# Optimization experiments

Hardware: AMD Instinct MI355X
Metric: run time of the kernel (lower is better)

The kernel has to match this reference:

```python
import jax, jax.numpy as jnp
import numpy as np

C, CH, H = 128, 32, 4  # c_in, c_hidden, n_head


def _layer_norm(x, w, b, eps=1e-5):
    mu = jnp.mean(x, axis=-1, keepdims=True)
    var = jnp.var(x, axis=-1, keepdims=True)
    return (x - mu) * jax.lax.rsqrt(var + eps) * w + b


def _tri_attn(x, ln_w, ln_b, wq, wk, wv, wz, wg, bg, wo, bo):
    # x: [B, I, J, C]; attention runs over J independently for each row I
    B, I, J, _ = x.shape
    x = _layer_norm(x, ln_w, ln_b)
    q = (x @ wq).reshape(B, I, J, H, CH) * (CH ** -0.5)
    k = (x @ wk).reshape(B, I, J, H, CH)
    v = (x @ wv).reshape(B, I, J, H, CH)
    # learned pairwise triangle bias: [B, I, J, H] -> [B, 1, H, I, J]
    tb = jnp.transpose(x @ wz, (0, 3, 1, 2))[:, None]
    scores = jnp.einsum('biqhd,bikhd->bihqk', q, k) + tb  # [B, I, H, J, J]
    a = jax.nn.softmax(scores, axis=-1)
    o = jnp.einsum('bihqk,bikhd->biqhd', a, v)
    g = jax.nn.sigmoid(x @ wg + bg).reshape(B, I, J, H, CH)
    o = (o * g).reshape(B, I, J, H * CH)
    return o @ wo + bo


def setup_inputs() -> dict:
    key = jax.random.key(0)
    ks = jax.random.split(key, 16)
    B, N = 1, 256
    inp = {'cmap': jax.random.normal(ks[0], (B, C, N, N), jnp.float32)}
    for i, p in enumerate(['s', 'e']):
        kq, kk, kv, kz, kg, ko = jax.random.split(ks[1 + i], 6)
        sd = 0.02
        inp[p + '_ln_w'] = jnp.ones((C,), jnp.float32)
        inp[p + '_ln_b'] = jnp.zeros((C,), jnp.float32)
        inp[p + '_wq'] = jax.random.normal(kq, (C, H * CH), jnp.float32) * sd
        inp[p + '_wk'] = jax.random.normal(kk, (C, H * CH), jnp.float32) * sd
        inp[p + '_wv'] = jax.random.normal(kv, (C, H * CH), jnp.float32) * sd
        inp[p + '_wz'] = jax.random.normal(kz, (C, H), jnp.float32) * sd
        inp[p + '_wg'] = jax.random.normal(kg, (C, H * CH), jnp.float32) * sd
        inp[p + '_bg'] = jnp.ones((H * CH,), jnp.float32)  # gating bias init = 1
        inp[p + '_wo'] = jax.random.normal(ko, (H * CH, C), jnp.float32) * sd
        inp[p + '_bo'] = jnp.zeros((C,), jnp.float32)
    return inp


def reference(cmap,
              s_ln_w, s_ln_b, s_wq, s_wk, s_wv, s_wz, s_wg, s_bg, s_wo, s_bo,
              e_ln_w, e_ln_b, e_wq, e_wk, e_wv, e_wz, e_wg, e_bg, e_wo, e_bo):
    # cmap: [B, C, I, J] -> channels last [B, I, J, C]
    x = jnp.transpose(cmap, (0, 2, 3, 1))
    # triangle attention around starting node (dropout is identity in eval)
    x = x + _tri_attn(x, s_ln_w, s_ln_b, s_wq, s_wk, s_wv, s_wz, s_wg, s_bg, s_wo, s_bo)
    # triangle attention around ending node: transpose I<->J, attend, transpose back
    xt = jnp.swapaxes(x, 1, 2)
    x = x + jnp.swapaxes(
        _tri_attn(xt, e_ln_w, e_ln_b, e_wq, e_wk, e_wv, e_wz, e_wg, e_bg, e_wo, e_bo), 1, 2)
    return jnp.transpose(x, (0, 3, 1, 2))
```

## Files before the change

kernel.cpp:

```cpp
#include <hip/hip_runtime.h>
#include <hip/hip_bf16.h>

#define NNX 256
#define CCX 128
#define HHX 4
#define CHDX 32
#define NIJ (NNX*NNX)

typedef __hip_bfloat16 bf16;
typedef __hip_bfloat162 bf162;
typedef __attribute__((ext_vector_type(8))) short short8v;
typedef __attribute__((ext_vector_type(4))) float float4v;
typedef __attribute__((ext_vector_type(4))) unsigned int uint4v;

__device__ __forceinline__ float4v MFMA(short8v a, short8v b, float4v c){
  return __builtin_amdgcn_mfma_f32_16x16x32_bf16(a, b, c, 0, 0, 0);
}

__device__ __forceinline__ unsigned pk2(float a, float b){
  unsigned short ua = __bfloat16_as_ushort(__float2bfloat16(a));
  unsigned short ub = __bfloat16_as_ushort(__float2bfloat16(b));
  return (unsigned)ua | ((unsigned)ub << 16);
}
__device__ __forceinline__ float ubf(unsigned short u){
  return __bfloat162float(__ushort_as_bfloat16(u));
}

__device__ __forceinline__ void load8bf16(const bf16* p, float* f){
  const bf162* p2 = (const bf162*)p;
  #pragma unroll
  for(int t=0;t<4;++t){ float2 xy = __bfloat1622float2(p2[t]); f[2*t]=xy.x; f[2*t+1]=xy.y; }
}

__global__ __launch_bounds__(256) void k_tin(const float* __restrict__ in, float* __restrict__ out){
  __shared__ float t[32][33];
  const int i = blockIdx.z, jt = blockIdx.x, ct = blockIdx.y;
  const int tx = threadIdx.x, ty = threadIdx.y;
  #pragma unroll
  for(int k=0;k<32;k+=8){
    int c = ct*32 + ty + k;
    t[ty+k][tx] = in[(size_t)c*NIJ + (size_t)i*NNX + jt*32 + tx];
  }
  __syncthreads();
  #pragma unroll
  for(int k=0;k<32;k+=8){
    int j = jt*32 + ty + k;
    out[((size_t)i*NNX + j)*CCX + ct*32 + tx] = t[tx][ty+k];
  }
}

__global__ __launch_bounds__(256) void k_tout(const float* __restrict__ x, float* __restrict__ out){
  __shared__ float t[32][33];
  const int i = blockIdx.z, jt = blockIdx.x, ct = blockIdx.y;
  const int tx = threadIdx.x, ty = threadIdx.y;
  #pragma unroll
  for(int k=0;k<32;k+=8){
    t[ty+k][tx] = x[((size_t)i*NNX + jt*32+ty+k)*CCX + ct*32 + tx];
  }
  __syncthreads();
  #pragma unroll
  for(int k=0;k<32;k+=8){
    out[(size_t)(ct*32+ty+k)*NIJ + (size_t)i*NNX + jt*32 + tx] = t[tx][ty+k];
  }
}

template<int TRANS>
__global__ __launch_bounds__(256) void k_lntb(const float* __restrict__ x,
    const float* __restrict__ w, const float* __restrict__ b,
    const float* __restrict__ wz, bf16* __restrict__ xln, float* __restrict__ tb2){
  const int r = blockIdx.x*4 + threadIdx.y;
  const int ii = r>>8, jj = r&255;
  const float* src = x + (size_t)(TRANS ? (jj*NNX+ii) : r)*CCX;
  const int c = threadIdx.x*2;
  float2 v = *(const float2*)(src+c);
  float s = v.x+v.y, s2 = v.x*v.x+v.y*v.y;
  #pragma unroll
  for(int off=32; off>0; off>>=1){ s += __shfl_xor(s,off); s2 += __shfl_xor(s2,off); }
  float mu = s*0.0078125f;
  float var = s2*0.0078125f - mu*mu;
  float rs = rsqrtf(var+1e-5f);
  float a0 = (v.x-mu)*rs*w[c]+b[c];
  float a1 = (v.y-mu)*rs*w[c+1]+b[c+1];
  bf162 hp; hp.x = __float2bfloat16(a0); hp.y = __float2bfloat16(a1);
  *(bf162*)(xln + (size_t)r*CCX + c) = hp;
  float acc[4];
  #pragma unroll
  for(int hh=0;hh<4;++hh) acc[hh] = a0*wz[c*4+hh] + a1*wz[(c+1)*4+hh];
  #pragma unroll
  for(int off=32; off>0; off>>=1){
    #pragma unroll
    for(int hh=0;hh<4;++hh) acc[hh] += __shfl_xor(acc[hh], off);
  }
  if(threadIdx.x==0){
    #pragma unroll
    for(int hh=0;hh<4;++hh) tb2[(size_t)hh*NIJ + r] = acc[hh];
  }
}

__global__ __launch_bounds__(256) void k_cvtw(const float* __restrict__ wq,
    const float* __restrict__ wk, const float* __restrict__ wv,
    const float* __restrict__ wg, const float* __restrict__ wo, bf16* __restrict__ wT){
  int idx = blockIdx.x*256 + threadIdx.x;
  if(idx < 65536){
    int n = idx >> 7, k = idx & 127;
    const float* W = (n<128)?wq:(n<256)?wk:(n<384)?wv:wg;
    wT[idx] = __float2bfloat16(W[k*CCX + (n&127)]);
  } else {
    int idx2 = idx - 65536;
    int n = idx2 >> 7, k = idx2 & 127;
    wT[idx] = __float2bfloat16(wo[k*CCX + n]);
  }
}

__global__ __launch_bounds__(256,2) void k_fattn(const bf16* __restrict__ xln,
    const bf16* __restrict__ wT, const float* __restrict__ bg,
    const float* __restrict__ tb2, bf16* __restrict__ op){
  __shared__ unsigned short Qs[256*40];
  __shared__ unsigned short Ks[256*40];
  __shared__ unsigned short Vt[32*256];
  const int id = blockIdx.x;
  const int i = id >> 2, h = id & 3;
  const int tid = threadIdx.x;
  const int w = tid >> 6, l = tid & 63;
  const int lq = l & 15, g = l >> 4;
  const int mb = w*64;

  short8v bx[4][4];
  #pragma unroll
  for(int ms=0; ms<4; ++ms){
    const size_t row = (size_t)i*NNX + mb + ms*16 + lq;
    #pragma unroll
    for(int kc=0; kc<4; ++kc)
      bx[ms][kc] = *(const short8v*)(xln + row*CCX + kc*32 + g*8);
  }
  float4v greg[2][4];
  char* qsb = (char*)Qs;
  char* ksb = (char*)Ks;
  char* vtb = (char*)Vt;
  #pragma unroll
  for(int mat=0; mat<4; ++mat){
    #pragma unroll
    for(int half=0; half<2; ++half){
      const int n0 = mat*128 + h*32 + half*16;
      float4v acc[4];
      #pragma unroll
      for(int ms=0; ms<4; ++ms) acc[ms] = (float4v)(0.f);
      #pragma unroll
      for(int kc=0; kc<4; ++kc){
        short8v aw = *(const short8v*)(wT + (size_t)(n0 + lq)*CCX + kc*32 + g*8);
        #pragma unroll
        for(int ms=0; ms<4; ++ms) acc[ms] = MFMA(aw, bx[ms][kc], acc[ms]);
      }
      if(mat==0){
        #pragma unroll
        for(int ms=0; ms<4; ++ms){
          const int row = mb + ms*16 + lq;
          uint2 pw; pw.x = pk2(acc[ms][0]*0.17677669529663687f, acc[ms][1]*0.17677669529663687f);
                    pw.y = pk2(acc[ms][2]*0.17677669529663687f, acc[ms][3]*0.17677669529663687f);
          *(uint2*)(qsb + (size_t)row*80 + half*32 + g*8) = pw;
        }
      } else if(mat==1){
        #pragma unroll
        for(int ms=0; ms<4; ++ms){
          const int row = mb + ms*16 + lq;
          uint2 pw; pw.x = pk2(acc[ms][0], acc[ms][1]);
                    pw.y = pk2(acc[ms][2], acc[ms][3]);
          *(uint2*)(ksb + (size_t)row*80 + half*32 + g*8) = pw;
        }
      } else if(mat==2){
        #pragma unroll
        for(int ms=0; ms<4; ++ms){
          const int k = mb + ms*16 + lq;
          const int j = k & 31;
          const int kap = (k & ~31) + 8*((j>>2)&3) + 4*((j>>4)&1) + (j&3);
          #pragma unroll
          for(int r=0; r<4; ++r){
            const int d = half*16 + 4*g + r;
            const int off = d*512 + ((2*kap) ^ ((d&7)<<4));
            *(unsigned short*)(vtb + off) = __bfloat16_as_ushort(__float2bfloat16(acc[ms][r]));
          }
        }
      } else {
        const float4 bg4 = *(const float4*)(bg + h*32 + half*16 + 4*g);
        #pragma unroll
        for(int ms=0; ms<4; ++ms){
          float4v t = acc[ms];
          t[0]+=bg4.x; t[1]+=bg4.y; t[2]+=bg4.z; t[3]+=bg4.w;
          greg[half][ms] = t;
        }
      }
    }
  }
  __syncthreads();

  bf16* obh = op + ((size_t)h*NIJ + (size_t)i*NNX)*CHDX;
  #pragma unroll 1
  for(int sub=0; sub<4; ++sub){
    const int q0 = mb + sub*16;
    const int q  = q0 + lq;
    short8v qf = *(const short8v*)(qsb + (size_t)q*80 + g*16);
    const float* tbq = tb2 + (size_t)h*NIJ + (size_t)q*NNX;
    float4v s[16];
    #pragma unroll
    for(int t=0;t<16;++t){
      short8v ak = *(const short8v*)(ksb + (size_t)(t*16 + lq)*80 + g*16);
      float4v bb = *(const float4v*)(tbq + t*16 + g*4);
      s[t] = MFMA(ak, qf, bb);
    }
    float m = -1e30f;
    #pragma unroll
    for(int t=0;t<16;++t)
      m = fmaxf(m, fmaxf(fmaxf(s[t][0], s[t][1]), fmaxf(s[t][2], s[t][3])));
    m = fmaxf(m, __shfl_xor(m,16));
    m = fmaxf(m, __shfl_xor(m,32));
    float lsum = 0.f;
    #pragma unroll
    for(int t=0;t<16;++t){
      #pragma unroll
      for(int r=0;r<4;++r){ float e = __expf(s[t][r]-m); s[t][r]=e; lsum+=e; }
    }
    lsum += __shfl_xor(lsum,16);
    lsum += __shfl_xor(lsum,32);
    const float linv = 1.0f/lsum;
    #pragma unroll
    for(int dt=0; dt<2; ++dt){
      float4v acc = (float4v)(0.f);
      #pragma unroll
      for(int c=0;c<8;++c){
        const int vrow = dt*16 + lq;
        short8v av = *(const short8v*)(vtb + (size_t)vrow*512 + ((16*g + 64*c) ^ ((vrow&7)<<4)));
        uint4 pb;
        pb.x = pk2(s[2*c][0],   s[2*c][1]);
        pb.y = pk2(s[2*c][2],   s[2*c][3]);
        pb.z = pk2(s[2*c+1][0], s[2*c+1][1]);
        pb.w = pk2(s[2*c+1][2], s[2*c+1][3]);
        short8v bp;
        bp[0]=(short)(pb.x&0xffff); bp[1]=(short)(pb.x>>16);
        bp[2]=(short)(pb.y&0xffff); bp[3]=(short)(pb.y>>16);
        bp[4]=(short)(pb.z&0xffff); bp[5]=(short)(pb.z>>16);
        bp[6]=(short)(pb.w&0xffff); bp[7]=(short)(pb.w>>16);
        acc = MFMA(av, bp, acc);
      }
      const float4v gg = greg[dt][sub];
      float o0 = acc[0]*linv / (1.f + __expf(-gg[0]));
      float o1 = acc[1]*linv / (1.f + __expf(-gg[1]));
      float o2 = acc[2]*linv / (1.f + __expf(-gg[2]));
      float o3 = acc[3]*linv / (1.f + __expf(-gg[3]));
      uint2 pw; pw.x = pk2(o0,o1); pw.y = pk2(o2,o3);
      *(uint2*)(ksb + (size_t)(mb + lq*4 + 2*dt + (g>>1))*80 + 64 + (g&1)*8) = pw;
    }
    {
      const int r2 = l >> 2, c2 = l & 3;
      uint4v ow = *(const uint4v*)(ksb + (size_t)(mb + r2*4 + c2)*80 + 64);
      __builtin_nontemporal_store(ow, (uint4v*)(obh + (size_t)(q0 + r2)*CHDX + c2*8));
    }
  }
}

template<int TRANS>
__global__ __launch_bounds__(256) void k_oprojm(const bf16* __restrict__ ob,
    const bf16* __restrict__ woT, const float* __restrict__ bo, float* __restrict__ x){
  const int tid = threadIdx.x;
  const int w = tid >> 6, l = tid & 63;
  const int lq = l & 15, g = l >> 4;
  const int mbase = blockIdx.x*128 + w*32;
  short8v bx[2][4];
  #pragma unroll
  for(int ms=0; ms<2; ++ms){
    const size_t mrow = mbase + ms*16 + lq;
    #pragma unroll
    for(int kc=0; kc<4; ++kc)
      bx[ms][kc] = *(const short8v*)(ob + ((size_t)kc*NIJ + mrow)*CHDX + g*8);
  }
  #pragma unroll
  for(int nj=0; nj<8; ++nj){
    float4v acc0 = (float4v)(0.f), acc1 = (float4v)(0.f);
    #pragma unroll
    for(int kc=0; kc<4; ++kc){
      short8v aw = *(const short8v*)(woT + (size_t)(nj*16 + lq)*CCX + kc*32 + g*8);
      acc0 = MFMA(aw, bx[0][kc], acc0);
      acc1 = MFMA(aw, bx[1][kc], acc1);
    }
    const int col = nj*16 + 4*g;
    const float4 bo4 = *(const float4*)(bo + col);
    #pragma unroll
    for(int ms=0; ms<2; ++ms){
      const int r = mbase + ms*16 + lq;
      const int ii = r>>8, jj = r&255;
      float* dst = x + (size_t)(TRANS ? (jj*NNX+ii) : r)*CCX + col;
      float4 xv = *(float4*)dst;
      xv.x += ((ms==0)?acc0[0]:acc1[0]) + bo4.x;
      xv.y += ((ms==0)?acc0[1]:acc1[1]) + bo4.y;
      xv.z += ((ms==0)?acc0[2]:acc1[2]) + bo4.z;
      xv.w += ((ms==0)?acc0[3]:acc1[3]) + bo4.w;
      *(float4*)dst = xv;
    }
  }
}

extern "C" void kernel_launch(void* const* d_in, const int* in_sizes, int n_in,
                              void* d_out, int out_size, void* d_ws, size_t ws_size,
                              hipStream_t stream){
  const float* cmap = (const float*)d_in[0];
  char* ws = (char*)d_ws;
  float* x   = (float*)(ws);
  bf16* xln  = (bf16*)(ws + 33554432);
  bf16* ob   = (bf16*)(ws + 50331648);
  float* tb2 = (float*)(ws + 117440512);
  bf16* wT   = (bf16*)d_out;
  bf16* woT  = wT + 65536;
  float* outp = (float*)d_out;

  k_tin<<<dim3(8,4,NNX), dim3(32,8), 0, stream>>>(cmap, x);

  for(int p=0;p<2;++p){
    const int b = 1 + 10*p;
    const float* lnw = (const float*)d_in[b+0];
    const float* lnb = (const float*)d_in[b+1];
    const float* wq  = (const float*)d_in[b+2];
    const float* wk  = (const float*)d_in[b+3];
    const float* wv  = (const float*)d_in[b+4];
    const float* wz  = (const float*)d_in[b+5];
    const float* wg  = (const float*)d_in[b+6];
    const float* bg  = (const float*)d_in[b+7];
    const float* wo  = (const float*)d_in[b+8];
    const float* bo  = (const float*)d_in[b+9];

    k_cvtw<<<320, 256, 0, stream>>>(wq, wk, wv, wg, wo, wT);

    if(p==0) k_lntb<0><<<NIJ/4, dim3(64,4), 0, stream>>>(x, lnw, lnb, wz, xln, tb2);
    else     k_lntb<1><<<NIJ/4, dim3(64,4), 0, stream>>>(x, lnw, lnb, wz, xln, tb2);

    k_fattn<<<1024, 256, 0, stream>>>(xln, wT, bg, tb2, ob);

    if(p==0) k_oprojm<0><<<NIJ/128, 256, 0, stream>>>(ob, woT, bo, x);
    else     k_oprojm<1><<<NIJ/128, 256, 0, stream>>>(ob, woT, bo, x);
  }

  k_tout<<<dim3(8,4,NNX), dim3(32,8), 0, stream>>>(x, outp);
}
```

Measured before the change: 240.0 us.

## Keep Q fragments in registers via shuffles, raise occupancy, reorder blocks by head

Removes the Q shared-memory buffer by building the Q MFMA operand fragments directly in registers with cross-lane shuffles. The gate values are stored packed as bf16 instead of fp32 to cut register use, and launch bounds go from 2 to 4 blocks per CU. Block indexing becomes head-major, so consecutive blocks share a head's bias plane, and s_setprio raises priority around the MFMA loops. The sub-tile loop is fully unrolled through a template. Risks include register spills at the higher occupancy target and slightly lower gate precision from the bf16 packing.

Result: slower. 250.3 us (+4.3%).

```diff
diff --git a/kernel.cpp b/kernel.cpp
--- a/kernel.cpp
+++ b/kernel.cpp
@@ -112,19 +112,93 @@
   }
 }
 
-__global__ __launch_bounds__(256,2) void k_fattn(const bf16* __restrict__ xln,
+template<int SUB>
+__device__ __forceinline__ void attn_sub(const int mb,
+    const int lq, const int g, const int l,
+    short8v qf, uint2 pgl, uint2 pgh,
+    char* ksb, const char* vtb, const float* tbq_base, bf16* __restrict__ obh){
+  const int q0 = mb + SUB*16;
+  const int q  = q0 + lq;
+  const float* tbq = tbq_base + (size_t)q*NNX;
+  float4v s[16];
+  __builtin_amdgcn_s_setprio(1);
+  #pragma unroll
+  for(int t=0;t<16;++t){
+    short8v ak = *(const short8v*)(ksb + (size_t)(t*16 + lq)*80 + g*16);
+    float4v bb = *(const float4v*)(tbq + t*16 + g*4);
+    s[t] = MFMA(ak, qf, bb);
+  }
+  __builtin_amdgcn_s_setprio(0);
+  float m = -1e30f;
+  #pragma unroll
+  for(int t=0;t<16;++t)
+    m = fmaxf(m, fmaxf(fmaxf(s[t][0], s[t][1]), fmaxf(s[t][2], s[t][3])));
+  m = fmaxf(m, __shfl_xor(m,16));
+  m = fmaxf(m, __shfl_xor(m,32));
+  float lsum = 0.f;
+  #pragma unroll
+  for(int t=0;t<16;++t){
+    #pragma unroll
+    for(int r=0;r<4;++r){ float e = __expf(s[t][r]-m); s[t][r]=e; lsum+=e; }
+  }
+  lsum += __shfl_xor(lsum,16);
+  lsum += __shfl_xor(lsum,32);
+  const float linv = 1.0f/lsum;
+  #pragma unroll
+  for(int dt=0; dt<2; ++dt){
+    float4v acc = (float4v)(0.f);
+    __builtin_amdgcn_s_setprio(1);
+    #pragma unroll
+    for(int c=0;c<8;++c){
+      const int vrow = dt*16 + lq;
+      short8v av = *(const short8v*)(vtb + (size_t)vrow*512 + ((16*g + 64*c) ^ ((vrow&7)<<4)));
+      uint4 pb;
+      pb.x = pk2(s[2*c][0],   s[2*c][1]);
+      pb.y = pk2(s[2*c][2],   s[2*c][3]);
+      pb.z = pk2(s[2*c+1][0], s[2*c+1][1]);
+      pb.w = pk2(s[2*c+1][2], s[2*c+1][3]);
+      short8v bp;
+      bp[0]=(short)(pb.x&0xffff); bp[1]=(short)(pb.x>>16);
+      bp[2]=(short)(pb.y&0xffff); bp[3]=(short)(pb.y>>16);
+      bp[4]=(short)(pb.z&0xffff); bp[5]=(short)(pb.z>>16);
+      bp[6]=(short)(pb.w&0xffff); bp[7]=(short)(pb.w>>16);
+      acc = MFMA(av, bp, acc);
+    }
+    __builtin_amdgcn_s_setprio(0);
+    const uint2 pg = dt ? pgh : pgl;
+    float g0 = ubf((unsigned short)(pg.x & 0xffff));
+    float g1 = ubf((unsigned short)(pg.x >> 16));
+    float g2 = ubf((unsigned short)(pg.y & 0xffff));
+    float g3 = ubf((unsigned short)(pg.y >> 16));
+    float o0 = acc[0]*linv / (1.f + __expf(-g0));
+    float o1 = acc[1]*linv / (1.f + __expf(-g1));
+    float o2 = acc[2]*linv / (1.f + __expf(-g2));
+    float o3 = acc[3]*linv / (1.f + __expf(-g3));
+    uint2 pw; pw.x = pk2(o0,o1); pw.y = pk2(o2,o3);
+    *(uint2*)(ksb + (size_t)(mb + lq*4 + 2*dt + (g>>1))*80 + 64 + (g&1)*8) = pw;
+  }
+  {
+    const int r2 = l >> 2, c2 = l & 3;
+    uint4v ow = *(const uint4v*)(ksb + (size_t)(mb + r2*4 + c2)*80 + 64);
+    __builtin_nontemporal_store(ow, (uint4v*)(obh + (size_t)(q0 + r2)*CHDX + c2*8));
+  }
+}
+
+__global__ __launch_bounds__(256,4) void k_fattn(const bf16* __restrict__ xln,
     const bf16* __restrict__ wT, const float* __restrict__ bg,
     const float* __restrict__ tb2, bf16* __restrict__ op){
-  __shared__ unsigned short Qs[256*40];
   __shared__ unsigned short Ks[256*40];
   __shared__ unsigned short Vt[32*256];
   const int id = blockIdx.x;
-  const int i = id >> 2, h = id & 3;
+  const int h = id >> 8, i = id & 255;
   const int tid = threadIdx.x;
   const int w = tid >> 6, l = tid & 63;
   const int lq = l & 15, g = l >> 4;
   const int mb = w*64;
 
+  char* ksb = (char*)Ks;
+  char* vtb = (char*)Vt;
+
   short8v bx[4][4];
   #pragma unroll
   for(int ms=0; ms<4; ++ms){
@@ -133,15 +207,15 @@
     for(int kc=0; kc<4; ++kc)
       bx[ms][kc] = *(const short8v*)(xln + row*CCX + kc*32 + g*8);
   }
-  float4v greg[2][4];
-  char* qsb = (char*)Qs;
-  char* ksb = (char*)Ks;
-  char* vtb = (char*)Vt;
-  #pragma unroll
-  for(int mat=0; mat<4; ++mat){
+
+  uint4v qfr[4];
+  uint2 pgl[4], pgh[4];
+
+  {
+    uint2 pqa[4][2];
     #pragma unroll
     for(int half=0; half<2; ++half){
-      const int n0 = mat*128 + h*32 + half*16;
+      const int n0 = h*32 + half*16;
       float4v acc[4];
       #pragma unroll
       for(int ms=0; ms<4; ++ms) acc[ms] = (float4v)(0.f);
@@ -151,110 +225,100 @@
         #pragma unroll
         for(int ms=0; ms<4; ++ms) acc[ms] = MFMA(aw, bx[ms][kc], acc[ms]);
       }
-      if(mat==0){
-        #pragma unroll
-        for(int ms=0; ms<4; ++ms){
-          const int row = mb + ms*16 + lq;
-          uint2 pw; pw.x = pk2(acc[ms][0]*0.17677669529663687f, acc[ms][1]*0.17677669529663687f);
-                    pw.y = pk2(acc[ms][2]*0.17677669529663687f, acc[ms][3]*0.17677669529663687f);
-          *(uint2*)(qsb + (size_t)row*80 + half*32 + g*8) = pw;
-        }
-      } else if(mat==1){
-        #pragma unroll
-        for(int ms=0; ms<4; ++ms){
-          const int row = mb + ms*16 + lq;
-          uint2 pw; pw.x = pk2(acc[ms][0], acc[ms][1]);
-                    pw.y = pk2(acc[ms][2], acc[ms][3]);
-          *(uint2*)(ksb + (size_t)row*80 + half*32 + g*8) = pw;
-        }
-      } else if(mat==2){
-        #pragma unroll
-        for(int ms=0; ms<4; ++ms){
-          const int k = mb + ms*16 + lq;
-          const int j = k & 31;
-          const int kap = (k & ~31) + 8*((j>>2)&3) + 4*((j>>4)&1) + (j&3);
-          #pragma unroll
-          for(int r=0; r<4; ++r){
-            const int d = half*16 + 4*g + r;
-            const int off = d*512 + ((2*kap) ^ ((d&7)<<4));
-            *(unsigned short*)(vtb + off) = __bfloat16_as_ushort(__float2bfloat16(acc[ms][r]));
-          }
-        }
-      } else {
-        const float4 bg4 = *(const float4*)(bg + h*32 + half*16 + 4*g);
-        #pragma unroll
-        for(int ms=0; ms<4; ++ms){
-          float4v t = acc[ms];
-          t[0]+=bg4.x; t[1]+=bg4.y; t[2]+=bg4.z; t[3]+=bg4.w;
-          greg[half][ms] = t;
-        }
+      #pragma unroll
+      for(int ms=0; ms<4; ++ms){
+        pqa[ms][half].x = pk2(acc[ms][0]*0.17677669529663687f, acc[ms][1]*0.17677669529663687f);
+        pqa[ms][half].y = pk2(acc[ms][2]*0.17677669529663687f, acc[ms][3]*0.17677669529663687f);
       }
     }
+    const int srcA = lq + 32*(g&1);
+    const int hsel = g >> 1;
+    #pragma unroll
+    for(int ms=0; ms<4; ++ms){
+      unsigned sx = hsel ? pqa[ms][1].x : pqa[ms][0].x;
+      unsigned sy = hsel ? pqa[ms][1].y : pqa[ms][0].y;
+      qfr[ms].x = __shfl(sx, srcA);
+      qfr[ms].y = __shfl(sy, srcA);
+      qfr[ms].z = __shfl(sx, srcA+16);
+      qfr[ms].w = __shfl(sy, srcA+16);
+    }
+  }
+
+  #pragma unroll
+  for(int half=0; half<2; ++half){
+    const int n0 = 128 + h*32 + half*16;
+    float4v acc[4];
+    #pragma unroll
+    for(int ms=0; ms<4; ++ms) acc[ms] = (float4v)(0.f);
+    #pragma unroll
+    for(int kc=0; kc<4; ++kc){
+      short8v aw = *(const short8v*)(wT + (size_t)(n0 + lq)*CCX + kc*32 + g*8);
+      #pragma unroll
+      for(int ms=0; ms<4; ++ms) acc[ms] = MFMA(aw, bx[ms][kc], acc[ms]);
+    }
+    #pragma unroll
+    for(int ms=0; ms<4; ++ms){
+      const int row = mb + ms*16 + lq;
+      uint2 pw; pw.x = pk2(acc[ms][0], acc[ms][1]);
+                pw.y = pk2(acc[ms][2], acc[ms][3]);
+      *(uint2*)(ksb + (size_t)row*80 + half*32 + g*8) = pw;
+    }
+  }
+
+  #pragma unroll
+  for(int half=0; half<2; ++half){
+    const int n0 = 256 + h*32 + half*16;
+    float4v acc[4];
+    #pragma unroll
+    for(int ms=0; ms<4; ++ms) acc[ms] = (float4v)(0.f);
+    #pragma unroll
+    for(int kc=0; kc<4; ++kc){
+      short8v aw = *(const short8v*)(wT + (size_t)(n0 + lq)*CCX + kc*32 + g*8);
+      #pragma unroll
+      for(int ms=0; ms<4; ++ms) acc[ms] = MFMA(aw, bx[ms][kc], acc[ms]);
+    }
+    #pragma unroll
+    for(int ms=0; ms<4; ++ms){
+      const int k = mb + ms*16 + lq;
+      const int j = k & 31;
+      const int kap = (k & ~31) + 8*((j>>2)&3) + 4*((j>>4)&1) + (j&3);
+      #pragma unroll
+      for(int r=0; r<4; ++r){
+        const int d = half*16 + 4*g + r;
+        const int off = d*512 + ((2*kap) ^ ((d&7)<<4));
+        *(unsigned short*)(vtb + off) = __bfloat16_as_ushort(__float2bfloat16(acc[ms][r]));
+      }
+    }
+  }
+
+  #pragma unroll
+  for(int half=0; half<2; ++half){
+    const int n0 = 384 + h*32 + half*16;
+    float4v acc[4];
+    #pragma unroll
+    for(int ms=0; ms<4; ++ms) acc[ms] = (float4v)(0.f);
+    #pragma unroll
+    for(int kc=0; kc<4; ++kc){
+      short8v aw = *(const short8v*)(wT + (size_t)(n0 + lq)*CCX + kc*32 + g*8);
+      #pragma unroll
+      for(int ms=0; ms<4; ++ms) acc[ms] = MFMA(aw, bx[ms][kc], acc[ms]);
+    }
+    const float4 bg4 = *(const float4*)(bg + h*32 + half*16 + 4*g);
+    #pragma unroll
+    for(int ms=0; ms<4; ++ms){
+      uint2 pw; pw.x = pk2(acc[ms][0]+bg4.x, acc[ms][1]+bg4.y);
+                pw.y = pk2(acc[ms][2]+bg4.z, acc[ms][3]+bg4.w);
+      if(half==0) pgl[ms] = pw; else pgh[ms] = pw;
+    }
   }
   __syncthreads();
 
   bf16* obh = op + ((size_t)h*NIJ + (size_t)i*NNX)*CHDX;
-  #pragma unroll 1
-  for(int sub=0; sub<4; ++sub){
-    const int q0 = mb + sub*16;
-    const int q  = q0 + lq;
-    short8v qf = *(const short8v*)(qsb + (size_t)q*80 + g*16);
-    const float* tbq = tb2 + (size_t)h*NIJ + (size_t)q*NNX;
-    float4v s[16];
-    #pragma unroll
-    for(int t=0;t<16;++t){
-      short8v ak = *(const short8v*)(ksb + (size_t)(t*16 + lq)*80 + g*16);
-      float4v bb = *(const float4v*)(tbq + t*16 + g*4);
-      s[t] = MFMA(ak, qf, bb);
-    }
-    float m = -1e30f;
-    #pragma unroll
-    for(int t=0;t<16;++t)
-      m = fmaxf(m, fmaxf(fmaxf(s[t][0], s[t][1]), fmaxf(s[t][2], s[t][3])));
-    m = fmaxf(m, __shfl_xor(m,16));
-    m = fmaxf(m, __shfl_xor(m,32));
-    float lsum = 0.f;
-    #pragma unroll
-    for(int t=0;t<16;++t){
-      #pragma unroll
-      for(int r=0;r<4;++r){ float e = __expf(s[t][r]-m); s[t][r]=e; lsum+=e; }
-    }
-    lsum += __shfl_xor(lsum,16);
-    lsum += __shfl_xor(lsum,32);
-    const float linv = 1.0f/lsum;
-    #pragma unroll
-    for(int dt=0; dt<2; ++dt){
-      float4v acc = (float4v)(0.f);
-      #pragma unroll
-      for(int c=0;c<8;++c){
-        const int vrow = dt*16 + lq;
-        short8v av = *(const short8v*)(vtb + (size_t)vrow*512 + ((16*g + 64*c) ^ ((vrow&7)<<4)));
-        uint4 pb;
-        pb.x = pk2(s[2*c][0],   s[2*c][1]);
-        pb.y = pk2(s[2*c][2],   s[2*c][3]);
-        pb.z = pk2(s[2*c+1][0], s[2*c+1][1]);
-        pb.w = pk2(s[2*c+1][2], s[2*c+1][3]);
-        short8v bp;
-        bp[0]=(short)(pb.x&0xffff); bp[1]=(short)(pb.x>>16);
-        bp[2]=(short)(pb.y&0xffff); bp[3]=(short)(pb.y>>16);
-        bp[4]=(short)(pb.z&0xffff); bp[5]=(short)(pb.z>>16);
-        bp[6]=(short)(pb.w&0xffff); bp[7]=(short)(pb.w>>16);
-        acc = MFMA(av, bp, acc);
-      }
-      const float4v gg = greg[dt][sub];
-      float o0 = acc[0]*linv / (1.f + __expf(-gg[0]));
-      float o1 = acc[1]*linv / (1.f + __expf(-gg[1]));
-      float o2 = acc[2]*linv / (1.f + __expf(-gg[2]));
-      float o3 = acc[3]*linv / (1.f + __expf(-gg[3]));
-      uint2 pw; pw.x = pk2(o0,o1); pw.y = pk2(o2,o3);
-      *(uint2*)(ksb + (size_t)(mb + lq*4 + 2*dt + (g>>1))*80 + 64 + (g&1)*8) = pw;
-    }
-    {
-      const int r2 = l >> 2, c2 = l & 3;
-      uint4v ow = *(const uint4v*)(ksb + (size_t)(mb + r2*4 + c2)*80 + 64);
-      __builtin_nontemporal_store(ow, (uint4v*)(obh + (size_t)(q0 + r2)*CHDX + c2*8));
-    }
-  }
+  const float* tbq_base = tb2 + (size_t)h*NIJ;
+  attn_sub<0>(mb, lq, g, l, __builtin_bit_cast(short8v, qfr[0]), pgl[0], pgh[0], ksb, vtb, tbq_base, obh);
+  attn_sub<1>(mb, lq, g, l, __builtin_bit_cast(short8v, qfr[1]), pgl[1], pgh[1], ksb, vtb, tbq_base, obh);
+  attn_sub<2>(mb, lq, g, l, __builtin_bit_cast(short8v, qfr[2]), pgl[2], pgh[2], ksb, vtb, tbq_base, obh);
+  attn_sub<3>(mb, lq, g, l, __builtin_bit_cast(short8v, qfr[3]), pgl[3], pgh[3], ksb, vtb, tbq_base, obh);
 }
 
 template<int TRANS>
```
